# Kernel optimization log

Measured on AMD Instinct MI355X. Metric: run time of the kernel, lower is better.

Reference implementation:

```python
import jax, jax.numpy as jnp
import numpy as np

N_ATOM, N_QUERY, KNN = 100000, 20000, 32
E = N_QUERY * KNN
HID, EDGE_F, HEADS = 128, 16, 8
D_HEAD = HID // HEADS
LN_EPS = 1e-5


def setup_inputs() -> dict:
    key = jax.random.key(0)
    ks = jax.random.split(key, 16)
    s = 1.0 / np.sqrt(HID)
    src = jax.random.randint(ks[0], (E,), 0, N_ATOM)
    dst = jnp.repeat(jnp.arange(N_QUERY), KNN)  # each query has KNN incoming edges
    return {
        "h_atom": jax.random.normal(ks[1], (N_ATOM, HID), jnp.float32),
        "h_query": jax.random.normal(ks[2], (N_QUERY, HID), jnp.float32),
        "edge_attr": jax.random.uniform(ks[3], (E, EDGE_F), jnp.float32),
        "W_q": jax.random.normal(ks[4], (HID, HID), jnp.float32) * s,
        "W_k": jax.random.normal(ks[5], (HID, HID), jnp.float32) * s,
        "W_v": jax.random.normal(ks[6], (HID, HID), jnp.float32) * s,
        "W_rbf": jax.random.normal(ks[7], (HEADS, EDGE_F), jnp.float32) * (1.0 / np.sqrt(EDGE_F)),
        "W1": jax.random.normal(ks[8], (HID, 2 * HID), jnp.float32) * (1.0 / np.sqrt(2 * HID)),
        "b1": jnp.zeros((HID,), jnp.float32),
        "W2": jax.random.normal(ks[9], (HID, HID), jnp.float32) * s,
        "b2": jnp.zeros((HID,), jnp.float32),
        "ln_gamma": jnp.ones((HID,), jnp.float32),
        "ln_beta": jnp.zeros((HID,), jnp.float32),
        "edge_index": jnp.stack([src, dst]),
        "n_query": N_QUERY,
    }


def reference(h_atom, h_query, edge_attr, W_q, W_k, W_v, W_rbf, W1, b1, W2, b2,
              ln_gamma, ln_beta, edge_index, n_query):
    src, dst = edge_index[0], edge_index[1]
    En = src.shape[0]
    # gather + project, per-edge multi-head Q/K/V  [E, H, d]
    Q = (h_query[dst] @ W_q.T).reshape(En, HEADS, D_HEAD)
    K = (h_atom[src] @ W_k.T).reshape(En, HEADS, D_HEAD)
    V = (h_atom[src] @ W_v.T).reshape(En, HEADS, D_HEAD)
    scores = jnp.einsum("ehd,ehd->eh", Q, K) / np.sqrt(D_HEAD) + edge_attr @ W_rbf.T  # [E,H]
    # segment softmax over edges sharing the same dst query, per head
    seg_max = jax.lax.stop_gradient(jax.ops.segment_max(scores, dst, num_segments=n_query))
    ex = jnp.exp(scores - seg_max[dst])
    denom = jax.ops.segment_sum(ex, dst, num_segments=n_query)
    alpha = ex / (denom[dst] + 1e-16)  # [E,H]
    # weighted scatter-add aggregation
    msgs = (alpha[:, :, None] * V).reshape(En, HID)
    agg = jax.ops.segment_sum(msgs, dst, num_segments=n_query)  # [Nq, HID]
    # update MLP + residual + LayerNorm
    z = jnp.concatenate([h_query, agg], axis=-1)
    delta = jax.nn.relu(z @ W1.T + b1) @ W2.T + b2
    y = h_query + delta
    mu = y.mean(-1, keepdims=True)
    var = y.var(-1, keepdims=True)
    return (y - mu) / jnp.sqrt(var + LN_EPS) * ln_gamma + ln_beta
```

## Files before the change

### kernel.cpp

```cpp
#include <hip/hip_runtime.h>
#include <hip/hip_bf16.h>
#include <math.h>

#define N_ATOM   100000
#define N_QUERY  20000
#define KNN      32

typedef __attribute__((ext_vector_type(8))) short  short8;
typedef __attribute__((ext_vector_type(4))) float  floatx4;
typedef __attribute__((ext_vector_type(2))) float  fx2;

static __device__ __forceinline__ unsigned short f2bf_bits(float f) {
  union { __hip_bfloat16 h; unsigned short u; } cv;
  cv.h = __float2bfloat16(f);
  return cv.u;
}
static __device__ __forceinline__ float bflo(unsigned int u) { return __uint_as_float(u << 16); }
static __device__ __forceinline__ float bfhi(unsigned int u) { return __uint_as_float(u & 0xffff0000u); }

__global__ void pack_all_kernel(const float* __restrict__ Wq, const float* __restrict__ Wk,
                                const float* __restrict__ Wv, const float* __restrict__ W1,
                                const float* __restrict__ W2,
                                unsigned short* __restrict__ WKVp, unsigned short* __restrict__ WQp,
                                unsigned short* __restrict__ W1p,  unsigned short* __restrict__ W2p) {
  int tid = blockIdx.x * blockDim.x + threadIdx.x;
  if (tid >= 98304) return;
  const float *Wa, *Wb; int nsplit, Kd, Nd; unsigned short* dst; float scale = 1.0f;
  int t = tid;
  if (t < 32768)      { Wa = Wk; Wb = Wv; nsplit = 128; Kd = 128; Nd = 256; dst = WKVp; }
  else if (t < 49152) { t -= 32768; Wa = Wq; Wb = Wq; nsplit = 128; Kd = 128; Nd = 128; dst = WQp; scale = 0.25f; }
  else if (t < 81920) { t -= 49152; Wa = W1; Wb = W1; nsplit = 128; Kd = 256; Nd = 128; dst = W1p; }
  else                { t -= 81920; Wa = W2; Wb = W2; nsplit = 128; Kd = 128; Nd = 128; dst = W2p; }
  int j    = t & 7;
  int lane = (t >> 3) & 63;
  int t2   = t >> 9;
  int NT   = Nd >> 4;
  int ntile = t2 % NT;
  int ktile = t2 / NT;
  int k = ktile * 32 + (lane >> 4) * 8 + j;
  int n = ntile * 16 + (lane & 15);
  float v = (n < nsplit) ? Wa[(size_t)n * Kd + k] : Wb[(size_t)(n - nsplit) * Kd + k];
  dst[t] = f2bf_bits(v * scale);
}

template<int KD, int NT, int EPI>
__global__ __launch_bounds__(256) void gemm_k(
    const float* __restrict__ A, const unsigned short* __restrict__ Bp, int M,
    unsigned short* __restrict__ outb, unsigned char* __restrict__ outp8) {
  constexpr int ND = NT * 16;
  constexpr int LDSB = (EPI == 3) ? 24576 : 16;
  __shared__ char lds[LDSB];
  const int l    = threadIdx.x & 63;
  const int w    = threadIdx.x >> 6;
  const int quad = l >> 4;
  const int col0 = l & 15;
  const int row0 = blockIdx.x * 64 + w * 16;
  int arow = row0 + col0;
  if (arow >= M) arow = M - 1;

  floatx4 acc[NT];
#pragma unroll
  for (int i = 0; i < NT; i++) acc[i] = (floatx4){0.f, 0.f, 0.f, 0.f};

  const float* aptr = A + (size_t)arow * KD + quad * 8;
#pragma unroll
  for (int k0 = 0; k0 < KD; k0 += 32) {
    floatx4 a0 = *(const floatx4*)(aptr + k0);
    floatx4 a1 = *(const floatx4*)(aptr + k0 + 4);
    short8 af;
    af[0] = (short)f2bf_bits(a0[0]); af[1] = (short)f2bf_bits(a0[1]);
    af[2] = (short)f2bf_bits(a0[2]); af[3] = (short)f2bf_bits(a0[3]);
    af[4] = (short)f2bf_bits(a1[0]); af[5] = (short)f2bf_bits(a1[1]);
    af[6] = (short)f2bf_bits(a1[2]); af[7] = (short)f2bf_bits(a1[3]);
    const unsigned short* bbase = Bp + (size_t)(k0 >> 5) * NT * 512 + l * 8;
#pragma unroll
    for (int nt = 0; nt < NT; nt++) {
      short8 bf = *(const short8*)(bbase + nt * 512);
      acc[nt] = __builtin_amdgcn_mfma_f32_16x16x32_bf16(af, bf, acc[nt], 0, 0, 0);
    }
  }

  if (EPI == 0) {
#pragma unroll
    for (int nt = 0; nt < NT; nt++) {
#pragma unroll
      for (int r = 0; r < 4; r++) {
        int row = row0 + quad * 4 + r;
        if (row < M) outb[(size_t)row * ND + nt * 16 + col0] = f2bf_bits(acc[nt][r]);
      }
    }
  } else {
#pragma unroll
    for (int nt = 0; nt < NT; nt++) {
#pragma unroll
      for (int r = 0; r < 4; r++) {
        int rl = w * 16 + quad * 4 + r;
        int c  = nt * 16 + col0;
        if (c < 128) {
          int pk = __builtin_amdgcn_cvt_pk_fp8_f32(acc[nt][r], acc[nt][r], 0, false);
          lds[rl * 128 + c] = (char)(pk & 0xff);
        } else {
          *(unsigned short*)&lds[8192 + rl * 256 + (c - 128) * 2] = f2bf_bits(acc[nt][r]);
        }
      }
    }
    __syncthreads();
    const int row0g = blockIdx.x * 64;
#pragma unroll
    for (int it = 0; it < 2; it++) {
      int off = threadIdx.x * 16 + it * 4096;
      if (row0g + (off >> 7) < M)
        *(float4*)(outp8 + (size_t)row0g * 128 + off) = *(const float4*)&lds[off];
    }
#pragma unroll
    for (int it = 0; it < 4; it++) {
      int off = threadIdx.x * 16 + it * 4096;
      if (row0g + (off >> 8) < M)
        *(float4*)((char*)outb + (size_t)row0g * 256 + off) = *(const float4*)&lds[8192 + off];
    }
  }
}

__global__ __launch_bounds__(256) void attn_kernel(
    const unsigned short* __restrict__ Qb,
    const unsigned char* __restrict__ Kp8,
    const unsigned short* __restrict__ Vb,
    const float* __restrict__ edge_attr,
    const float* __restrict__ Wrbf,
    const int* __restrict__ src,
    float* __restrict__ Agg) {
  const int l  = threadIdx.x & 63;
  const int w  = threadIdx.x >> 6;
  const int q  = blockIdx.x * 4 + w;
  const int hw = l >> 5;
  const int m  = l & 31;
  const int c  = m & 3;

  uint2 qu = *(const uint2*)(Qb + (size_t)q * 128 + 4 * m);
  float qd0 = bflo(qu.x), qd1 = bfhi(qu.x), qd2 = bflo(qu.y), qd3 = bfhi(qu.y);
  float4 wr = *(const float4*)(Wrbf + (m >> 2) * 16 + 4 * c);

  const int e0 = q * KNN;
  int srcj = (l < KNN) ? src[e0 + l] : 0;

  float lsum = 0.f, a0 = 0.f, a1 = 0.f, a2 = 0.f, a3 = 0.f;
#pragma unroll 4
  for (int t = 0; t < 16; t++) {
    int e = hw * 16 + t;
    int s = __shfl(srcj, e, 64);
    unsigned int ku = *(const unsigned int*)(Kp8 + (size_t)s * 128 + 4 * m);
    uint2 vu = *(const uint2*)(Vb + (size_t)s * 128 + 4 * m);
    float4 ea = *(const float4*)(edge_attr + (size_t)(e0 + e) * 16 + 4 * c);
    fx2 k01 = __builtin_amdgcn_cvt_pk_f32_fp8((int)ku, false);
    fx2 k23 = __builtin_amdgcn_cvt_pk_f32_fp8((int)ku, true);
    float part = qd0 * k01[0] + qd1 * k01[1] + qd2 * k23[0] + qd3 * k23[1]
               + wr.x * ea.x + wr.y * ea.y + wr.z * ea.z + wr.w * ea.w;
    part += __shfl_xor(part, 1, 64);
    part += __shfl_xor(part, 2, 64);
    float p = __expf(part);
    lsum += p;
    a0 += p * bflo(vu.x); a1 += p * bfhi(vu.x);
    a2 += p * bflo(vu.y); a3 += p * bfhi(vu.y);
  }
  a0 += __shfl_xor(a0, 32, 64);
  a1 += __shfl_xor(a1, 32, 64);
  a2 += __shfl_xor(a2, 32, 64);
  a3 += __shfl_xor(a3, 32, 64);
  lsum += __shfl_xor(lsum, 32, 64);
  float inv = 1.f / (lsum + 1e-16f);
  if (hw == 0) {
    float4 o; o.x = a0 * inv; o.y = a1 * inv; o.z = a2 * inv; o.w = a3 * inv;
    *(float4*)(Agg + (size_t)q * 128 + 4 * m) = o;
  }
}

__global__ __launch_bounds__(256) void mlp_kernel(
    const float* __restrict__ h_query, const float* __restrict__ Agg,
    const unsigned short* __restrict__ W1p, const unsigned short* __restrict__ W2p,
    const float* __restrict__ b1, const float* __restrict__ b2,
    const float* __restrict__ gamma, const float* __restrict__ beta,
    float* __restrict__ out) {
  constexpr int M = N_QUERY;
  constexpr int STRIDE = 136;
  __shared__ unsigned short hid[64 * STRIDE];

  const int l    = threadIdx.x & 63;
  const int w    = threadIdx.x >> 6;
  const int quad = l >> 4;
  const int col0 = l & 15;
  const int row0 = blockIdx.x * 64 + w * 16;
  int arow = row0 + col0;
  if (arow >= M) arow = M - 1;

  floatx4 acc[8];
#pragma unroll
  for (int i = 0; i < 8; i++) acc[i] = (floatx4){0.f, 0.f, 0.f, 0.f};
#pragma unroll
  for (int k0 = 0; k0 < 256; k0 += 32) {
    const float* sp = (k0 < 128) ? (h_query + (size_t)arow * 128 + k0)
                                 : (Agg + (size_t)arow * 128 + (k0 - 128));
    floatx4 a0 = *(const floatx4*)(sp + quad * 8);
    floatx4 a1 = *(const floatx4*)(sp + quad * 8 + 4);
    short8 af;
    af[0] = (short)f2bf_bits(a0[0]); af[1] = (short)f2bf_bits(a0[1]);
    af[2] = (short)f2bf_bits(a0[2]); af[3] = (short)f2bf_bits(a0[3]);
    af[4] = (short)f2bf_bits(a1[0]); af[5] = (short)f2bf_bits(a1[1]);
    af[6] = (short)f2bf_bits(a1[2]); af[7] = (short)f2bf_bits(a1[3]);
    const unsigned short* bbase = W1p + (size_t)(k0 >> 5) * 8 * 512 + l * 8;
#pragma unroll
    for (int nt = 0; nt < 8; nt++) {
      short8 bf = *(const short8*)(bbase + nt * 512);
      acc[nt] = __builtin_amdgcn_mfma_f32_16x16x32_bf16(af, bf, acc[nt], 0, 0, 0);
    }
  }
#pragma unroll
  for (int nt = 0; nt < 8; nt++) {
#pragma unroll
    for (int r = 0; r < 4; r++) {
      int rl = w * 16 + quad * 4 + r;
      float v = acc[nt][r] + b1[nt * 16 + col0];
      hid[rl * STRIDE + nt * 16 + col0] = f2bf_bits(fmaxf(v, 0.f));
    }
  }
  __syncthreads();

  floatx4 acc2[8];
#pragma unroll
  for (int i = 0; i < 8; i++) acc2[i] = (floatx4){0.f, 0.f, 0.f, 0.f};
  const int rloc = w * 16 + col0;
#pragma unroll
  for (int k0 = 0; k0 < 128; k0 += 32) {
    short8 af = *(const short8*)(hid + rloc * STRIDE + k0 + quad * 8);
    const unsigned short* bbase = W2p + (size_t)(k0 >> 5) * 8 * 512 + l * 8;
#pragma unroll
    for (int nt = 0; nt < 8; nt++) {
      short8 bf = *(const short8*)(bbase + nt * 512);
      acc2[nt] = __builtin_amdgcn_mfma_f32_16x16x32_bf16(af, bf, acc2[nt], 0, 0, 0);
    }
  }

#pragma unroll
  for (int r = 0; r < 4; r++) {
    int row = row0 + quad * 4 + r;
    int rr  = row < M ? row : M - 1;
    float v[8];
    float s1 = 0.f, s2 = 0.f;
#pragma unroll
    for (int nt = 0; nt < 8; nt++) {
      int c = nt * 16 + col0;
      v[nt] = acc2[nt][r] + b2[c] + h_query[(size_t)rr * 128 + c];
      s1 += v[nt];
    }
    s1 += __shfl_xor(s1, 1, 64); s1 += __shfl_xor(s1, 2, 64);
    s1 += __shfl_xor(s1, 4, 64); s1 += __shfl_xor(s1, 8, 64);
#pragma unroll
    for (int nt = 0; nt < 8; nt++) s2 += v[nt] * v[nt];
    s2 += __shfl_xor(s2, 1, 64); s2 += __shfl_xor(s2, 2, 64);
    s2 += __shfl_xor(s2, 4, 64); s2 += __shfl_xor(s2, 8, 64);
    float mean = s1 * (1.0f / 128.0f);
    float var  = s2 * (1.0f / 128.0f) - mean * mean;
    float rstd = rsqrtf(var + 1e-5f);
    if (row < M) {
#pragma unroll
      for (int nt = 0; nt < 8; nt++) {
        int c = nt * 16 + col0;
        out[(size_t)row * 128 + c] = (v[nt] - mean) * rstd * gamma[c] + beta[c];
      }
    }
  }
}

extern "C" void kernel_launch(void* const* d_in, const int* in_sizes, int n_in,
                              void* d_out, int out_size, void* d_ws, size_t ws_size,
                              hipStream_t stream) {
  const float* h_atom    = (const float*)d_in[0];
  const float* h_query   = (const float*)d_in[1];
  const float* edge_attr = (const float*)d_in[2];
  const float* W_q  = (const float*)d_in[3];
  const float* W_k  = (const float*)d_in[4];
  const float* W_v  = (const float*)d_in[5];
  const float* Wrbf = (const float*)d_in[6];
  const float* W1   = (const float*)d_in[7];
  const float* b1   = (const float*)d_in[8];
  const float* W2   = (const float*)d_in[9];
  const float* b2   = (const float*)d_in[10];
  const float* ln_g = (const float*)d_in[11];
  const float* ln_b = (const float*)d_in[12];
  const int* edge_index = (const int*)d_in[13];
  float* out = (float*)d_out;

  char* ws = (char*)d_ws;
  unsigned char*  Kp8 = (unsigned char*)(ws);
  unsigned short* Vb  = (unsigned short*)(ws + 12800000);
  unsigned short* Qb  = (unsigned short*)(ws + 38400000);
  float* Agg          = (float*)(ws + 43520000);
  unsigned short* WKVp = (unsigned short*)(ws + 53760000);
  unsigned short* WQp  = WKVp + 32768;
  unsigned short* W1p  = WQp  + 16384;
  unsigned short* W2p  = W1p  + 32768;

  pack_all_kernel<<<(98304 + 255) / 256, 256, 0, stream>>>(
      W_q, W_k, W_v, W1, W2, WKVp, WQp, W1p, W2p);

  gemm_k<128, 16, 3><<<(N_ATOM + 63) / 64, 256, 0, stream>>>(
      h_atom, WKVp, N_ATOM, Vb, Kp8);
  gemm_k<128, 8, 0><<<(N_QUERY + 63) / 64, 256, 0, stream>>>(
      h_query, WQp, N_QUERY, Qb, nullptr);
  attn_kernel<<<N_QUERY / 4, 256, 0, stream>>>(Qb, Kp8, Vb, edge_attr, Wrbf, edge_index, Agg);
  mlp_kernel<<<(N_QUERY + 63) / 64, 256, 0, stream>>>(
      h_query, Agg, W1p, W2p, b1, b2, ln_g, ln_b, out);
}
```

Baseline: 251.5 us.

## Remap attention lanes to one head per lane over eight edges

Reorganizes the attention kernel so each lane owns a full head (16 dims) for one of eight edges per pass, instead of four dims per lane across sixteen sequential edges. Score reduction no longer needs intra-edge shuffles, loads become wider (uint4 K/V rows, full edge_attr rows), and the loop shrinks to four fully unrolled passes. In exchange it uses many more registers (16 accumulators, 16 q and 16 weight values), does redundant edge_attr loads per head lane, and needs a larger cross-lane reduction of 17 values over three shuffle stages.

```diff
diff --git a/kernel.cpp b/kernel.cpp
--- a/kernel.cpp
+++ b/kernel.cpp
@@ -129,48 +129,97 @@
     const float* __restrict__ Wrbf,
     const int* __restrict__ src,
     float* __restrict__ Agg) {
-  const int l  = threadIdx.x & 63;
-  const int w  = threadIdx.x >> 6;
-  const int q  = blockIdx.x * 4 + w;
-  const int hw = l >> 5;
-  const int m  = l & 31;
-  const int c  = m & 3;
-
-  uint2 qu = *(const uint2*)(Qb + (size_t)q * 128 + 4 * m);
-  float qd0 = bflo(qu.x), qd1 = bfhi(qu.x), qd2 = bflo(qu.y), qd3 = bfhi(qu.y);
-  float4 wr = *(const float4*)(Wrbf + (m >> 2) * 16 + 4 * c);
+  const int l = threadIdx.x & 63;
+  const int w = threadIdx.x >> 6;
+  const int q = blockIdx.x * 4 + w;
+  const int j = l >> 3;
+  const int h = l & 7;
 
   const int e0 = q * KNN;
   int srcj = (l < KNN) ? src[e0 + l] : 0;
 
-  float lsum = 0.f, a0 = 0.f, a1 = 0.f, a2 = 0.f, a3 = 0.f;
-#pragma unroll 4
-  for (int t = 0; t < 16; t++) {
-    int e = hw * 16 + t;
+  float qd[16];
+  {
+    const unsigned int* qp = (const unsigned int*)(Qb + (size_t)q * 128 + h * 16);
+#pragma unroll
+    for (int i = 0; i < 8; i++) {
+      unsigned int u = qp[i];
+      qd[2 * i] = bflo(u); qd[2 * i + 1] = bfhi(u);
+    }
+  }
+  float wr[16];
+  {
+    const float* wp = Wrbf + h * 16;
+#pragma unroll
+    for (int i = 0; i < 16; i++) wr[i] = wp[i];
+  }
+
+  float acc[16];
+#pragma unroll
+  for (int i = 0; i < 16; i++) acc[i] = 0.f;
+  float lsum = 0.f;
+
+#pragma unroll
+  for (int p = 0; p < 4; p++) {
+    const int e = p * 8 + j;
     int s = __shfl(srcj, e, 64);
-    unsigned int ku = *(const unsigned int*)(Kp8 + (size_t)s * 128 + 4 * m);
-    uint2 vu = *(const uint2*)(Vb + (size_t)s * 128 + 4 * m);
-    float4 ea = *(const float4*)(edge_attr + (size_t)(e0 + e) * 16 + 4 * c);
-    fx2 k01 = __builtin_amdgcn_cvt_pk_f32_fp8((int)ku, false);
-    fx2 k23 = __builtin_amdgcn_cvt_pk_f32_fp8((int)ku, true);
-    float part = qd0 * k01[0] + qd1 * k01[1] + qd2 * k23[0] + qd3 * k23[1]
-               + wr.x * ea.x + wr.y * ea.y + wr.z * ea.z + wr.w * ea.w;
-    part += __shfl_xor(part, 1, 64);
-    part += __shfl_xor(part, 2, 64);
-    float p = __expf(part);
-    lsum += p;
-    a0 += p * bflo(vu.x); a1 += p * bfhi(vu.x);
-    a2 += p * bflo(vu.y); a3 += p * bfhi(vu.y);
-  }
-  a0 += __shfl_xor(a0, 32, 64);
-  a1 += __shfl_xor(a1, 32, 64);
-  a2 += __shfl_xor(a2, 32, 64);
-  a3 += __shfl_xor(a3, 32, 64);
-  lsum += __shfl_xor(lsum, 32, 64);
+    uint4 kq = *(const uint4*)(Kp8 + (size_t)s * 128 + h * 16);
+    const uint4* vp = (const uint4*)(Vb + ((size_t)s * 128 + h * 16));
+    uint4 v0 = vp[0], v1 = vp[1];
+    const float4* ep = (const float4*)(edge_attr + (size_t)(e0 + e) * 16);
+    float4 ea0 = ep[0], ea1 = ep[1], ea2 = ep[2], ea3 = ep[3];
+
+    float kd = 0.f;
+    {
+      fx2 f0, f1;
+      f0 = __builtin_amdgcn_cvt_pk_f32_fp8((int)kq.x, false);
+      f1 = __builtin_amdgcn_cvt_pk_f32_fp8((int)kq.x, true);
+      kd += qd[0] * f0[0] + qd[1] * f0[1] + qd[2] * f1[0] + qd[3] * f1[1];
+      f0 = __builtin_amdgcn_cvt_pk_f32_fp8((int)kq.y, false);
+      f1 = __builtin_amdgcn_cvt_pk_f32_fp8((int)kq.y, true);
+      kd += qd[4] * f0[0] + qd[5] * f0[1] + qd[6] * f1[0] + qd[7] * f1[1];
+      f0 = __builtin_amdgcn_cvt_pk_f32_fp8((int)kq.z, false);
+      f1 = __builtin_amdgcn_cvt_pk_f32_fp8((int)kq.z, true);
+      kd += qd[8] * f0[0] + qd[9] * f0[1] + qd[10] * f1[0] + qd[11] * f1[1];
+      f0 = __builtin_amdgcn_cvt_pk_f32_fp8((int)kq.w, false);
+      f1 = __builtin_amdgcn_cvt_pk_f32_fp8((int)kq.w, true);
+      kd += qd[12] * f0[0] + qd[13] * f0[1] + qd[14] * f1[0] + qd[15] * f1[1];
+    }
+    float ed = wr[0]*ea0.x + wr[1]*ea0.y + wr[2]*ea0.z + wr[3]*ea0.w
+             + wr[4]*ea1.x + wr[5]*ea1.y + wr[6]*ea1.z + wr[7]*ea1.w
+             + wr[8]*ea2.x + wr[9]*ea2.y + wr[10]*ea2.z + wr[11]*ea2.w
+             + wr[12]*ea3.x + wr[13]*ea3.y + wr[14]*ea3.z + wr[15]*ea3.w;
+
+    float pe = __expf(kd + ed);
+    lsum += pe;
+    acc[0]  += pe * bflo(v0.x); acc[1]  += pe * bfhi(v0.x);
+    acc[2]  += pe * bflo(v0.y); acc[3]  += pe * bfhi(v0.y);
+    acc[4]  += pe * bflo(v0.z); acc[5]  += pe * bfhi(v0.z);
+    acc[6]  += pe * bflo(v0.w); acc[7]  += pe * bfhi(v0.w);
+    acc[8]  += pe * bflo(v1.x); acc[9]  += pe * bfhi(v1.x);
+    acc[10] += pe * bflo(v1.y); acc[11] += pe * bfhi(v1.y);
+    acc[12] += pe * bflo(v1.z); acc[13] += pe * bfhi(v1.z);
+    acc[14] += pe * bflo(v1.w); acc[15] += pe * bfhi(v1.w);
+  }
+
+#pragma unroll
+  for (int mask = 8; mask <= 32; mask <<= 1) {
+    lsum += __shfl_xor(lsum, mask, 64);
+#pragma unroll
+    for (int i = 0; i < 16; i++) acc[i] += __shfl_xor(acc[i], mask, 64);
+  }
   float inv = 1.f / (lsum + 1e-16f);
-  if (hw == 0) {
-    float4 o; o.x = a0 * inv; o.y = a1 * inv; o.z = a2 * inv; o.w = a3 * inv;
-    *(float4*)(Agg + (size_t)q * 128 + 4 * m) = o;
+  float* dst = Agg + (size_t)q * 128 + h * 16;
+  if (j == 0) {
+    float4 o0 = {acc[0] * inv, acc[1] * inv, acc[2] * inv, acc[3] * inv};
+    float4 o1 = {acc[4] * inv, acc[5] * inv, acc[6] * inv, acc[7] * inv};
+    *(float4*)(dst)     = o0;
+    *(float4*)(dst + 4) = o1;
+  } else if (j == 1) {
+    float4 o2 = {acc[8] * inv, acc[9] * inv, acc[10] * inv, acc[11] * inv};
+    float4 o3 = {acc[12] * inv, acc[13] * inv, acc[14] * inv, acc[15] * inv};
+    *(float4*)(dst + 8)  = o2;
+    *(float4*)(dst + 12) = o3;
   }
 }
 
```

Measured after the change: 238.0 us. 1.06x faster.
